# Performance work log

Hardware: AMD Instinct MI355X
Metric: run time of the kernel (lower is better)

## Reference

```python
import jax, jax.numpy as jnp
import numpy as np
from jax import lax

B, T, D = 4, 4096, 1024
H, d = 4, 64
EPS = 1e-6

def pos_unit(x):
    # positive feature map (elu+1) normalized to unit L2 norm along feature dim
    p = jax.nn.elu(x) + 1.0
    return p / (jnp.linalg.norm(p, axis=-1, keepdims=True) + EPS)

def setup_inputs() -> dict:
    key = jax.random.key(0)
    ks = jax.random.split(key, 5)
    s_in = 1.0 / np.sqrt(D)
    s_hd = 1.0 / np.sqrt(H * d)
    return {
        "x": jax.random.normal(ks[0], (B, T, D), dtype=jnp.float32),
        "Wq": jax.random.normal(ks[1], (H * d, D), dtype=jnp.float32) * s_in,
        "Wk": jax.random.normal(ks[2], (H * d, D), dtype=jnp.float32) * s_in,
        "Wv": jax.random.normal(ks[3], (H * d, D), dtype=jnp.float32) * s_in,
        "Wo": jax.random.normal(ks[4], (D, H * d), dtype=jnp.float32) * s_hd,
    }

def reference(x, Wq, Wk, Wv, Wo):
    Bx, Tx, Dx = x.shape
    q = (x @ Wq.T).reshape(Bx, Tx, H, d)
    k = (x @ Wk.T).reshape(Bx, Tx, H, d)
    v = (x @ Wv.T).reshape(Bx, Tx, H, d)
    q = pos_unit(q)
    k = pos_unit(k)
    # time-major for scan: [T, B, H, d]
    qT = jnp.transpose(q, (1, 0, 2, 3))
    kT = jnp.transpose(k, (1, 0, 2, 3))
    vT = jnp.transpose(v, (1, 0, 2, 3))
    kv0 = jnp.zeros((Bx, H, d, d), dtype=x.dtype)  # [B,H,j,d]
    kc0 = jnp.zeros((Bx, H, d), dtype=x.dtype)

    def step(carry, inp):
        kv_cum, k_cum = carry
        qt, kt, vt = inp  # each [B,H,d]
        kv_cum = kv_cum + jnp.einsum('bhd,bhj->bhjd', kt, vt)
        k_cum = k_cum + kt
        num = jnp.einsum('bhd,bhjd->bhj', qt, kv_cum)
        den = jnp.einsum('bhd,bhd->bh', qt, k_cum)[..., None] + EPS
        return (kv_cum, k_cum), num / den

    (kv_f, kc_f), yT = lax.scan(step, (kv0, kc0), (qT, kT, vT))
    y = jnp.transpose(yT, (1, 0, 2, 3)).reshape(Bx, Tx, H * d)
    y = y @ Wo.T
    return y, kv_f, kc_f
```

## Files before the change

### kernel.cpp

```cpp
#include <hip/hip_runtime.h>
#include <hip/hip_bf16.h>
#include <math.h>

#define T_SEQ   4096
#define NB      4
#define NH      4
#define DH      64
#define DM      1024
#define MR      16384
#define NQKV    768
#define CH      64
#define NCH     64
#define SST     4160
#define BHN     16

typedef __attribute__((ext_vector_type(4))) float          f32x4;
typedef __attribute__((ext_vector_type(8))) short          s16x8;
typedef __attribute__((ext_vector_type(4))) unsigned short u16x4;

__device__ __forceinline__ float bf2f(unsigned short u) {
  union { unsigned int i; float f; } c; c.i = ((unsigned int)u) << 16; return c.f;
}
__device__ __forceinline__ unsigned short f2bf(float f) {
  union { float f; unsigned int i; } c; c.f = f;
  unsigned int i = c.i;
  return (unsigned short)((i + 0x7fffu + ((i >> 16) & 1u)) >> 16);
}
__device__ __forceinline__ s16x8 pack8(f32x4 lo, f32x4 hi) {
  s16x8 r;
  r[0] = (short)f2bf(lo.x); r[1] = (short)f2bf(lo.y);
  r[2] = (short)f2bf(lo.z); r[3] = (short)f2bf(lo.w);
  r[4] = (short)f2bf(hi.x); r[5] = (short)f2bf(hi.y);
  r[6] = (short)f2bf(hi.z); r[7] = (short)f2bf(hi.w);
  return r;
}
__device__ __forceinline__ void gl_lds16(const unsigned short* g, unsigned short* l) {
  __builtin_amdgcn_global_load_lds(
      (const __attribute__((address_space(1))) unsigned int*)g,
      (__attribute__((address_space(3))) unsigned int*)l, 16, 0, 0);
}

__global__ __launch_bounds__(256) void convert_kernel(
    const float* __restrict__ X,
    const float* __restrict__ Wq, const float* __restrict__ Wk,
    const float* __restrict__ Wv,
    unsigned short* __restrict__ Xb, unsigned short* __restrict__ Wb)
{
  const long long NX = 16777216LL;
  const long long NW = 786432LL;
  const long long total = NX + NW;
  const long long stride = (long long)gridDim.x * 256 * 8;
  for (long long i = ((long long)blockIdx.x * 256 + threadIdx.x) * 8;
       i < total; i += stride) {
    const float* src;
    unsigned short* dst;
    if (i < NX) { src = X + i; dst = Xb + i; }
    else {
      const long long e = i - NX;
      const int w = (int)(e >> 18);
      const long long rr = e & 262143LL;
      src = (w == 0 ? Wq : w == 1 ? Wk : Wv) + rr;
      dst = Wb + e;
    }
    const f32x4 lo = *(const f32x4*)src;
    const f32x4 hi = *(const f32x4*)(src + 4);
    *(s16x8*)dst = pack8(lo, hi);
  }
}

__global__ __launch_bounds__(256) void convert_wo_kernel(
    const float* __restrict__ Wo, unsigned short* __restrict__ WoB)
{
  const int i = (blockIdx.x * 256 + threadIdx.x) * 8;
  const f32x4 lo = *(const f32x4*)(Wo + i);
  const f32x4 hi = *(const f32x4*)(Wo + i + 4);
  *(s16x8*)(WoB + i) = pack8(lo, hi);
}

__global__ __launch_bounds__(256, 2) void gemm_qkv_kernel(
    const unsigned short* __restrict__ Xb,
    const unsigned short* __restrict__ Wb,
    unsigned short* __restrict__ C)
{
  constexpr int K = DM;
  constexpr int N = NQKV;
  __shared__ __align__(16) unsigned short sA[2][128 * 32];
  __shared__ __align__(16) unsigned short sB[2][128 * 32];

  const int tid  = threadIdx.x;
  const int wave = tid >> 6;
  const int lane = tid & 63;
  const int quad = lane >> 4;
  const int l16  = lane & 15;
  const int wm = (wave >> 1) * 64;
  const int wn = (wave & 1) * 64;

  const int row0 = blockIdx.x * 128;
  const int bn   = blockIdx.y;
  const int srow = tid >> 2;
  const int scol = ((tid & 3) ^ (srow & 3)) * 8;
  const unsigned short* Ag = Xb + (size_t)(row0     + srow) * K + scol;
  const unsigned short* Bg = Wb + (size_t)(bn * 128 + srow) * K + scol;

  const int ra = (quad ^ (l16 & 3)) * 8;

  f32x4 acc[4][4];
  #pragma unroll
  for (int i = 0; i < 4; i++)
    #pragma unroll
    for (int j = 0; j < 4; j++) acc[i][j] = (f32x4){0.f, 0.f, 0.f, 0.f};

  gl_lds16(Ag,                       &sA[0][tid * 8]);
  gl_lds16(Ag + (size_t)64 * K,      &sA[0][tid * 8 + 2048]);
  gl_lds16(Bg,                       &sB[0][tid * 8]);
  gl_lds16(Bg + (size_t)64 * K,      &sB[0][tid * 8 + 2048]);
  gl_lds16(Ag + 32,                  &sA[1][tid * 8]);
  gl_lds16(Ag + 32 + (size_t)64 * K, &sA[1][tid * 8 + 2048]);
  gl_lds16(Bg + 32,                  &sB[1][tid * 8]);
  gl_lds16(Bg + 32 + (size_t)64 * K, &sB[1][tid * 8 + 2048]);
  asm volatile("s_waitcnt vmcnt(4)" ::: "memory");
  __builtin_amdgcn_sched_barrier(0);
  __builtin_amdgcn_s_barrier();

  int cur = 0;
  for (int kt = 0; kt < K; kt += 32) {
    s16x8 af[4], bw[4];
    #pragma unroll
    for (int i = 0; i < 4; i++)
      af[i] = *(const s16x8*)(&sA[cur][(wm + i * 16 + l16) * 32 + ra]);
    #pragma unroll
    for (int j = 0; j < 4; j++)
      bw[j] = *(const s16x8*)(&sB[cur][(wn + j * 16 + l16) * 32 + ra]);
    asm volatile("s_waitcnt lgkmcnt(0)" ::: "memory");
    __builtin_amdgcn_sched_barrier(0);
    __builtin_amdgcn_s_barrier();
    {
      const int ktp = (kt + 64 < K) ? (kt + 64) : (K - 32);
      gl_lds16(Ag + ktp,                  &sA[cur][tid * 8]);
      gl_lds16(Ag + ktp + (size_t)64 * K, &sA[cur][tid * 8 + 2048]);
      gl_lds16(Bg + ktp,                  &sB[cur][tid * 8]);
      gl_lds16(Bg + ktp + (size_t)64 * K, &sB[cur][tid * 8 + 2048]);
    }
    #pragma unroll
    for (int i = 0; i < 4; i++)
      #pragma unroll
      for (int j = 0; j < 4; j++)
        acc[i][j] = __builtin_amdgcn_mfma_f32_16x16x32_bf16(af[i], bw[j], acc[i][j], 0, 0, 0);
    asm volatile("s_waitcnt vmcnt(4)" ::: "memory");
    __builtin_amdgcn_sched_barrier(0);
    __builtin_amdgcn_s_barrier();
    cur ^= 1;
  }

  const int colb = bn * 128 + wn;
  if (bn < 4) {
    #pragma unroll
    for (int i = 0; i < 4; i++) {
      const int r = row0 + wm + i * 16 + quad * 4;
      #pragma unroll
      for (int g = 0; g < 4; g++) {
        float p[4];
        float ss = 0.f;
        #pragma unroll
        for (int j = 0; j < 4; j++) {
          const float a = acc[i][j][g];
          p[j] = a > 0.f ? a + 1.f : __expf(a);
          ss += p[j] * p[j];
        }
        ss += __shfl_xor(ss, 1, 64);
        ss += __shfl_xor(ss, 2, 64);
        ss += __shfl_xor(ss, 4, 64);
        ss += __shfl_xor(ss, 8, 64);
        const float inv = 1.f / (sqrtf(ss) + 1e-6f);
        #pragma unroll
        for (int j = 0; j < 4; j++)
          C[(size_t)(r + g) * N + colb + j * 16 + l16] = f2bf(p[j] * inv);
      }
    }
  } else {
    #pragma unroll
    for (int i = 0; i < 4; i++) {
      const int r = row0 + wm + i * 16 + quad * 4;
      #pragma unroll
      for (int j = 0; j < 4; j++) {
        const int cc = colb + j * 16 + l16;
        #pragma unroll
        for (int g = 0; g < 4; g++)
          C[(size_t)(r + g) * N + cc] = f2bf(acc[i][j][g]);
      }
    }
  }
}

__global__ __launch_bounds__(256, 2) void gemm_out_kernel(
    const unsigned short* __restrict__ Y,
    const unsigned short* __restrict__ WoB,
    float* __restrict__ Out)
{
  constexpr int K = 256;
  constexpr int N = DM;
  __shared__ __align__(16) unsigned short sA[128 * 32];
  __shared__ __align__(16) unsigned short sB[128 * 32];

  const int tid  = threadIdx.x;
  const int wave = tid >> 6;
  const int lane = tid & 63;
  const int quad = lane >> 4;
  const int l16  = lane & 15;
  const int wm = (wave >> 1) * 64;
  const int wn = (wave & 1) * 64;

  const int row0  = blockIdx.x * 128;
  const int bcol0 = blockIdx.y * 128;

  const int srow = tid >> 2;
  const int scol = ((tid & 3) ^ (srow & 3)) * 8;
  const unsigned short* Ag = Y   + (size_t)(row0  + srow) * K + scol;
  const unsigned short* Bg = WoB + (size_t)(bcol0 + srow) * K + scol;
  unsigned short* sAp = sA + tid * 8;
  unsigned short* sBp = sB + tid * 8;

  const int ra = (quad ^ (l16 & 3)) * 8;

  f32x4 acc[4][4];
  #pragma unroll
  for (int i = 0; i < 4; i++)
    #pragma unroll
    for (int j = 0; j < 4; j++) acc[i][j] = (f32x4){0.f, 0.f, 0.f, 0.f};

  for (int kt = 0; kt < K; kt += 32) {
    __syncthreads();
    gl_lds16(Ag + kt,                  sAp);
    gl_lds16(Ag + kt + (size_t)64 * K, sAp + 2048);
    gl_lds16(Bg + kt,                  sBp);
    gl_lds16(Bg + kt + (size_t)64 * K, sBp + 2048);
    __syncthreads();
    s16x8 af[4], bw[4];
    #pragma unroll
    for (int i = 0; i < 4; i++)
      af[i] = *(const s16x8*)(sA + (wm + i * 16 + l16) * 32 + ra);
    #pragma unroll
    for (int j = 0; j < 4; j++)
      bw[j] = *(const s16x8*)(sB + (wn + j * 16 + l16) * 32 + ra);
    #pragma unroll
    for (int i = 0; i < 4; i++)
      #pragma unroll
      for (int j = 0; j < 4; j++)
        acc[i][j] = __builtin_amdgcn_mfma_f32_16x16x32_bf16(af[i], bw[j], acc[i][j], 0, 0, 0);
  }

  #pragma unroll
  for (int i = 0; i < 4; i++) {
    const int r = row0 + wm + i * 16 + quad * 4;
    #pragma unroll
    for (int j = 0; j < 4; j++) {
      const int cc = bcol0 + wn + j * 16 + l16;
      #pragma unroll
      for (int g = 0; g < 4; g++)
        Out[(size_t)(r + g) * N + cc] = acc[i][j][g];
    }
  }
}

__global__ __launch_bounds__(256) void chunk_sums_kernel(
    const unsigned short* __restrict__ qkv,
    float* __restrict__ cs)
{
  const int blk = blockIdx.x;
  const int bh = blk >> 6, c = blk & 63;
  const int b = bh >> 2, h = bh & 3;
  __shared__ __align__(16) unsigned short sKt[64 * 64];
  __shared__ __align__(16) unsigned short sVt[64 * 64];
  __shared__ float sPart[4 * 64];
  const int wave = threadIdx.x >> 6, lane = threadIdx.x & 63;
  const int quad = lane >> 4, l16 = lane & 15;
  const size_t rowbase = ((size_t)b * T_SEQ + (size_t)c * CH) * NQKV + h * DH;

  float kacc = 0.f;
  #pragma unroll 4
  for (int tt = 0; tt < 16; tt++) {
    const int t = tt * 4 + wave;
    const unsigned short* r = qkv + rowbase + (size_t)t * NQKV;
    const unsigned short ku = r[256 + lane];
    const unsigned short vu = r[512 + lane];
    kacc += bf2f(ku);
    const int sw = (lane & 7) << 3;
    sKt[lane * 64 + (t ^ sw)] = ku;
    sVt[lane * 64 + (t ^ sw)] = vu;
  }
  sPart[wave * 64 + lane] = kacc;
  __syncthreads();

  const int wr = (wave >> 1) * 32;
  const int wc = (wave & 1) * 32;
  f32x4 acc[2][2];
  #pragma unroll
  for (int i = 0; i < 2; i++)
    #pragma unroll
    for (int j = 0; j < 2; j++) acc[i][j] = (f32x4){0.f, 0.f, 0.f, 0.f};

  #pragma unroll
  for (int ks = 0; ks < 2; ks++) {
    const int grp = ks * 4 + quad;
    s16x8 ak[2], bv[2];
    #pragma unroll
    for (int i = 0; i < 2; i++) {
      const int rk = wr + i * 16 + l16;
      ak[i] = *(const s16x8*)(sKt + rk * 64 + ((grp ^ (rk & 7)) << 3));
    }
    #pragma unroll
    for (int j = 0; j < 2; j++) {
      const int rj = wc + j * 16 + l16;
      bv[j] = *(const s16x8*)(sVt + rj * 64 + ((grp ^ (rj & 7)) << 3));
    }
    #pragma unroll
    for (int i = 0; i < 2; i++)
      #pragma unroll
      for (int j = 0; j < 2; j++)
        acc[i][j] = __builtin_amdgcn_mfma_f32_16x16x32_bf16(ak[i], bv[j], acc[i][j], 0, 0, 0);
  }

  float* o = cs + (size_t)blk * SST;
  #pragma unroll
  for (int i = 0; i < 2; i++)
    #pragma unroll
    for (int j = 0; j < 2; j++)
      #pragma unroll
      for (int g = 0; g < 4; g++) {
        const int dd = wr + i * 16 + quad * 4 + g;
        const int jj = wc + j * 16 + l16;
        o[dd * 64 + jj] = acc[i][j][g];
      }
  if (threadIdx.x < 64)
    o[4096 + threadIdx.x] = sPart[threadIdx.x] + sPart[64 + threadIdx.x]
                          + sPart[128 + threadIdx.x] + sPart[192 + threadIdx.x];
}

__global__ __launch_bounds__(256) void scan_kernel(
    float* __restrict__ cs, float* __restrict__ outTail)
{
  const int gid = blockIdx.x * 256 + threadIdx.x;
  const int bh = gid / SST;
  const int e  = gid - bh * SST;
  float run = 0.f;
  size_t idx = (size_t)bh * NCH * SST + e;
  for (int c = 0; c < NCH; c++, idx += SST) {
    const float v = cs[idx];
    cs[idx] = run;
    run += v;
  }
  if (e < 4096) {
    const int dd = e >> 6, j = e & 63;
    outTail[(size_t)bh * 4096 + j * 64 + dd] = run;
  } else {
    const int dd = e - 4096;
    outTail[BHN * 4096 + (size_t)bh * 64 + dd] = run;
  }
}

__global__ __launch_bounds__(256, 4) void chunk_out_kernel(
    const unsigned short* __restrict__ qkv,
    const float* __restrict__ st,
    unsigned short* __restrict__ yatt)
{
  const int blk = blockIdx.x;
  const int bh = blk >> 6;
  const int c  = blk & 63;
  const int b = bh >> 2, h = bh & 3;

  __shared__ __align__(16) unsigned short sQ [64 * 64];
  __shared__ __align__(16) unsigned short sKA[64 * 64];
  __shared__ __align__(16) unsigned short sVt[64 * 64];
  __shared__ __align__(16) unsigned short sSt[64 * 64];
  __shared__ float sKc[64];
  __shared__ float sDen[64];

  const int tid  = threadIdx.x;
  const int wave = tid >> 6, lane = tid & 63;
  const int quad = lane >> 4, l16 = lane & 15;
  const size_t rowbase = ((size_t)b * T_SEQ + (size_t)c * CH) * NQKV + h * DH;

  #pragma unroll
  for (int p = 0; p < 2; p++) {
    const int e  = p * 2048 + tid * 8;
    const int t  = e >> 6;
    const int c0 = e & 56;
    const int sc = c0 ^ ((t & 7) << 3);
    const unsigned short* src = qkv + rowbase + (size_t)t * NQKV + sc;
    gl_lds16(src,       sQ  + e);
    gl_lds16(src + 256, sKA + e);
  }
  #pragma unroll 4
  for (int tt = 0; tt < 16; tt++) {
    const int t = tt * 4 + wave;
    sVt[lane * 64 + (t ^ ((lane & 7) << 3))] =
        qkv[rowbase + (size_t)t * NQKV + 512 + lane];
  }
  const float* stp = st + (size_t)blk * SST;
  for (int i = tid; i < 1024; i += 256) {
    const f32x4 s4 = ((const f32x4*)stp)[i];
    const int d = i >> 4, j0 = (i & 15) << 2;
    #pragma unroll
    for (int g = 0; g < 4; g++) {
      const int j = j0 + g;
      sSt[j * 64 + (d ^ ((j & 7) << 3))] = f2bf(s4[g]);
    }
  }
  if (tid < 64) sKc[tid] = stp[4096 + tid];
  __syncthreads();

  const int wr = (wave >> 1) * 32;
  const int wc = (wave & 1) * 32;

  f32x4 accA[2][2];
  #pragma unroll
  for (int i = 0; i < 2; i++)
    #pragma unroll
    for (int j = 0; j < 2; j++) accA[i][j] = (f32x4){0.f, 0.f, 0.f, 0.f};

  #pragma unroll
  for (int ks = 0; ks < 2; ks++) {
    const int grp = ks * 4 + quad;
    s16x8 aq[2], bk[2];
    #pragma unroll
    for (int i = 0; i < 2; i++) {
      const int rq = wr + i * 16 + l16;
      aq[i] = *(const s16x8*)(sQ + rq * 64 + ((grp ^ (rq & 7)) << 3));
    }
    #pragma unroll
    for (int j = 0; j < 2; j++) {
      const int rk = wc + j * 16 + l16;
      bk[j] = *(const s16x8*)(sKA + rk * 64 + ((grp ^ (rk & 7)) << 3));
    }
    #pragma unroll
    for (int i = 0; i < 2; i++)
      #pragma unroll
      for (int j = 0; j < 2; j++)
        accA[i][j] = __builtin_amdgcn_mfma_f32_16x16x32_bf16(aq[i], bk[j], accA[i][j], 0, 0, 0);
  }
  __syncthreads();

  #pragma unroll
  for (int i = 0; i < 2; i++)
    #pragma unroll
    for (int j = 0; j < 2; j++)
      #pragma unroll
      for (int g = 0; g < 4; g++) {
        const int t = wr + i * 16 + quad * 4 + g;
        const int s = wc + j * 16 + l16;
        const float av = (s <= t) ? accA[i][j][g] : 0.f;
        sKA[t * 64 + (s ^ ((t & 7) << 3))] = f2bf(av);
      }
  __syncthreads();

  {
    const int t = tid >> 2, p = tid & 3;
    const int sw = (t & 7) << 3;
    float s = 0.f;
    #pragma unroll
    for (int e = 0; e < 16; e++) {
      const int d = p * 16 + e;
      s += bf2f(sKA[t * 64 + d]);
      s += bf2f(sQ[t * 64 + (d ^ sw)]) * sKc[d];
    }
    s += __shfl_xor(s, 1, 64);
    s += __shfl_xor(s, 2, 64);
    if (p == 0) sDen[t] = s + 1e-6f;
  }
  __syncthreads();

  f32x4 acc[2][2];
  #pragma unroll
  for (int i = 0; i < 2; i++)
    #pragma unroll
    for (int j = 0; j < 2; j++) acc[i][j] = (f32x4){0.f, 0.f, 0.f, 0.f};

  #pragma unroll
  for (int ks = 0; ks < 2; ks++) {
    const int grp = ks * 4 + quad;
    s16x8 aq[2], bs[2];
    #pragma unroll
    for (int i = 0; i < 2; i++) {
      const int rq = wr + i * 16 + l16;
      aq[i] = *(const s16x8*)(sQ + rq * 64 + ((grp ^ (rq & 7)) << 3));
    }
    #pragma unroll
    for (int j = 0; j < 2; j++) {
      const int rj = wc + j * 16 + l16;
      bs[j] = *(const s16x8*)(sSt + rj * 64 + ((grp ^ (rj & 7)) << 3));
    }
    #pragma unroll
    for (int i = 0; i < 2; i++)
      #pragma unroll
      for (int j = 0; j < 2; j++)
        acc[i][j] = __builtin_amdgcn_mfma_f32_16x16x32_bf16(aq[i], bs[j], acc[i][j], 0, 0, 0);
  }
  #pragma unroll
  for (int ks = 0; ks < 2; ks++) {
    const int grp = ks * 4 + quad;
    s16x8 aa[2], bv[2];
    #pragma unroll
    for (int i = 0; i < 2; i++) {
      const int rt = wr + i * 16 + l16;
      aa[i] = *(const s16x8*)(sKA + rt * 64 + ((grp ^ (rt & 7)) << 3));
    }
    #pragma unroll
    for (int j = 0; j < 2; j++) {
      const int rj = wc + j * 16 + l16;
      bv[j] = *(const s16x8*)(sVt + rj * 64 + ((grp ^ (rj & 7)) << 3));
    }
    #pragma unroll
    for (int i = 0; i < 2; i++)
      #pragma unroll
      for (int j = 0; j < 2; j++)
        acc[i][j] = __builtin_amdgcn_mfma_f32_16x16x32_bf16(aa[i], bv[j], acc[i][j], 0, 0, 0);
  }

  #pragma unroll
  for (int i = 0; i < 2; i++)
    #pragma unroll
    for (int g = 0; g < 4; g++) {
      const int t = wr + i * 16 + quad * 4 + g;
      const float inv = 1.f / sDen[t];
      #pragma unroll
      for (int j = 0; j < 2; j++) {
        const int jj = wc + j * 16 + l16;
        const size_t o = ((size_t)b * T_SEQ + (size_t)c * CH + t) * 256 + h * 64 + jj;
        yatt[o] = f2bf(acc[i][j][g] * inv);
      }
    }
}

extern "C" void kernel_launch(void* const* d_in, const int* in_sizes, int n_in,
                              void* d_out, int out_size, void* d_ws, size_t ws_size,
                              hipStream_t stream) {
  const float* X  = (const float*)d_in[0];
  const float* Wq = (const float*)d_in[1];
  const float* Wk = (const float*)d_in[2];
  const float* Wv = (const float*)d_in[3];
  const float* Wo = (const float*)d_in[4];
  float* out = (float*)d_out;

  unsigned short* qkvb = (unsigned short*)d_out;
  unsigned short* Xb   = (unsigned short*)((char*)d_out + 25165824ull);
  unsigned short* Wb   = Xb + 16777216;
  float* outTail = out + 16777216;
  float*          cs   = (float*)d_ws;
  unsigned short* yatt = (unsigned short*)((char*)d_ws + 17039360ull);
  unsigned short* WoB  = (unsigned short*)d_ws;

  convert_kernel   <<<4096,         256, 0, stream>>>(X, Wq, Wk, Wv, Xb, Wb);
  gemm_qkv_kernel  <<<dim3(128, 6), 256, 0, stream>>>(Xb, Wb, qkvb);
  chunk_sums_kernel<<<BHN * NCH,    256, 0, stream>>>(qkvb, cs);
  scan_kernel      <<<(BHN * SST) / 256, 256, 0, stream>>>(cs, outTail);
  chunk_out_kernel <<<BHN * NCH,    256, 0, stream>>>(qkvb, cs, yatt);
  convert_wo_kernel<<<128,          256, 0, stream>>>(Wo, WoB);
  gemm_out_kernel  <<<dim3(128, 8), 256, 0, stream>>>(yatt, WoB, out);
}
```

Baseline: 196.6 us.

## Enlarge QKV GEMM tiles to 256x256x64 with 512 threads and block swizzle

Restructures the QKV projection GEMM from 128x128 tiles with K-step 32 and 4 waves to 256x256 tiles with K-step 64 and 8 waves. Each wave now computes a 128x64 sub-tile. The grid becomes a 1D launch of 192 blocks, swizzled so neighbouring blocks share rows. The larger tiles are meant to raise operand reuse and cut global and LDS traffic per FLOP, and setprio is raised around the MFMA section. In exchange, shared memory grows to 128KB per block, register pressure rises with 32 accumulators per thread, and 192 blocks may leave the 256 CUs underfilled.

```diff
diff --git a/kernel.cpp b/kernel.cpp
--- a/kernel.cpp
+++ b/kernel.cpp
@@ -77,86 +77,110 @@
   *(s16x8*)(WoB + i) = pack8(lo, hi);
 }
 
-__global__ __launch_bounds__(256, 2) void gemm_qkv_kernel(
+__global__ __launch_bounds__(512, 2) void gemm_qkv_kernel(
     const unsigned short* __restrict__ Xb,
     const unsigned short* __restrict__ Wb,
     unsigned short* __restrict__ C)
 {
   constexpr int K = DM;
   constexpr int N = NQKV;
-  __shared__ __align__(16) unsigned short sA[2][128 * 32];
-  __shared__ __align__(16) unsigned short sB[2][128 * 32];
+  __shared__ __align__(16) unsigned short sA[2][256 * 64];
+  __shared__ __align__(16) unsigned short sB[2][256 * 64];
 
   const int tid  = threadIdx.x;
   const int wave = tid >> 6;
   const int lane = tid & 63;
   const int quad = lane >> 4;
   const int l16  = lane & 15;
-  const int wm = (wave >> 1) * 64;
-  const int wn = (wave & 1) * 64;
-
-  const int row0 = blockIdx.x * 128;
-  const int bn   = blockIdx.y;
-  const int srow = tid >> 2;
-  const int scol = ((tid & 3) ^ (srow & 3)) * 8;
-  const unsigned short* Ag = Xb + (size_t)(row0     + srow) * K + scol;
-  const unsigned short* Bg = Wb + (size_t)(bn * 128 + srow) * K + scol;
-
-  const int ra = (quad ^ (l16 & 3)) * 8;
-
-  f32x4 acc[4][4];
-  #pragma unroll
-  for (int i = 0; i < 4; i++)
+  const int wr = (wave >> 2) * 128;
+  const int wc = (wave & 3) * 64;
+
+  const int orig = blockIdx.x;
+  const int swz  = (orig & 7) * 24 + (orig >> 3);
+  const int bx   = swz / 3;
+  const int bn   = swz % 3;
+  const int row0 = bx * 256;
+
+  const unsigned short* Ab = Xb + (size_t)row0 * K;
+  const unsigned short* Bb = Wb + (size_t)(bn * 256) * K;
+
+  const int srow = tid >> 3;
+  const int sg   = tid & 7;
+  const int ssc  = (sg ^ (srow & 7)) << 3;
+
+  f32x4 acc[8][4];
+  #pragma unroll
+  for (int i = 0; i < 8; i++)
     #pragma unroll
     for (int j = 0; j < 4; j++) acc[i][j] = (f32x4){0.f, 0.f, 0.f, 0.f};
 
-  gl_lds16(Ag,                       &sA[0][tid * 8]);
-  gl_lds16(Ag + (size_t)64 * K,      &sA[0][tid * 8 + 2048]);
-  gl_lds16(Bg,                       &sB[0][tid * 8]);
-  gl_lds16(Bg + (size_t)64 * K,      &sB[0][tid * 8 + 2048]);
-  gl_lds16(Ag + 32,                  &sA[1][tid * 8]);
-  gl_lds16(Ag + 32 + (size_t)64 * K, &sA[1][tid * 8 + 2048]);
-  gl_lds16(Bg + 32,                  &sB[1][tid * 8]);
-  gl_lds16(Bg + 32 + (size_t)64 * K, &sB[1][tid * 8 + 2048]);
-  asm volatile("s_waitcnt vmcnt(4)" ::: "memory");
+#define STAGE_QKV(c, kt)                                                      \
+  {                                                                           \
+    _Pragma("unroll")                                                         \
+    for (int p = 0; p < 4; p++)                                               \
+      gl_lds16(Ab + (size_t)(p * 64 + srow) * K + (kt) + ssc,                 \
+               &sA[c][p * 4096 + tid * 8]);                                   \
+    _Pragma("unroll")                                                         \
+    for (int p = 0; p < 4; p++)                                               \
+      gl_lds16(Bb + (size_t)(p * 64 + srow) * K + (kt) + ssc,                 \
+               &sB[c][p * 4096 + tid * 8]);                                   \
+  }
+
+  STAGE_QKV(0, 0);
+  STAGE_QKV(1, 64);
+  asm volatile("s_waitcnt vmcnt(8)" ::: "memory");
   __builtin_amdgcn_sched_barrier(0);
   __builtin_amdgcn_s_barrier();
 
   int cur = 0;
-  for (int kt = 0; kt < K; kt += 32) {
-    s16x8 af[4], bw[4];
-    #pragma unroll
-    for (int i = 0; i < 4; i++)
-      af[i] = *(const s16x8*)(&sA[cur][(wm + i * 16 + l16) * 32 + ra]);
+  for (int kt = 0; kt < K; kt += 64) {
+    s16x8 bwf[4][2];
     #pragma unroll
     for (int j = 0; j < 4; j++)
-      bw[j] = *(const s16x8*)(&sB[cur][(wn + j * 16 + l16) * 32 + ra]);
+      #pragma unroll
+      for (int ks = 0; ks < 2; ks++) {
+        const int r = wc + j * 16 + l16;
+        bwf[j][ks] = *(const s16x8*)(&sB[cur][r * 64 + (((ks * 4 + quad) ^ (r & 7)) << 3)]);
+      }
+    __builtin_amdgcn_s_setprio(1);
+    #pragma unroll
+    for (int ph = 0; ph < 4; ph++) {
+      s16x8 afp[2][2];
+      #pragma unroll
+      for (int ii = 0; ii < 2; ii++)
+        #pragma unroll
+        for (int ks = 0; ks < 2; ks++) {
+          const int r = wr + (ph * 2 + ii) * 16 + l16;
+          afp[ii][ks] = *(const s16x8*)(&sA[cur][r * 64 + (((ks * 4 + quad) ^ (r & 7)) << 3)]);
+        }
+      #pragma unroll
+      for (int ii = 0; ii < 2; ii++)
+        #pragma unroll
+        for (int j = 0; j < 4; j++) {
+          acc[ph * 2 + ii][j] = __builtin_amdgcn_mfma_f32_16x16x32_bf16(
+              afp[ii][0], bwf[j][0], acc[ph * 2 + ii][j], 0, 0, 0);
+          acc[ph * 2 + ii][j] = __builtin_amdgcn_mfma_f32_16x16x32_bf16(
+              afp[ii][1], bwf[j][1], acc[ph * 2 + ii][j], 0, 0, 0);
+        }
+    }
+    __builtin_amdgcn_s_setprio(0);
     asm volatile("s_waitcnt lgkmcnt(0)" ::: "memory");
     __builtin_amdgcn_sched_barrier(0);
     __builtin_amdgcn_s_barrier();
-    {
-      const int ktp = (kt + 64 < K) ? (kt + 64) : (K - 32);
-      gl_lds16(Ag + ktp,                  &sA[cur][tid * 8]);
-      gl_lds16(Ag + ktp + (size_t)64 * K, &sA[cur][tid * 8 + 2048]);
-      gl_lds16(Bg + ktp,                  &sB[cur][tid * 8]);
-      gl_lds16(Bg + ktp + (size_t)64 * K, &sB[cur][tid * 8 + 2048]);
-    }
-    #pragma unroll
-    for (int i = 0; i < 4; i++)
-      #pragma unroll
-      for (int j = 0; j < 4; j++)
-        acc[i][j] = __builtin_amdgcn_mfma_f32_16x16x32_bf16(af[i], bw[j], acc[i][j], 0, 0, 0);
-    asm volatile("s_waitcnt vmcnt(4)" ::: "memory");
+    const int ktp = (kt + 128 < K) ? (kt + 128) : (K - 64);
+    STAGE_QKV(cur, ktp);
+    asm volatile("s_waitcnt vmcnt(8)" ::: "memory");
     __builtin_amdgcn_sched_barrier(0);
     __builtin_amdgcn_s_barrier();
     cur ^= 1;
   }
-
-  const int colb = bn * 128 + wn;
-  if (bn < 4) {
-    #pragma unroll
-    for (int i = 0; i < 4; i++) {
-      const int r = row0 + wm + i * 16 + quad * 4;
+#undef STAGE_QKV
+
+  const int colb = bn * 256 + wc;
+  if (bn < 2) {
+    #pragma unroll
+    for (int i = 0; i < 8; i++) {
+      const int r = row0 + wr + i * 16 + quad * 4;
       #pragma unroll
       for (int g = 0; g < 4; g++) {
         float p[4];
@@ -179,8 +203,8 @@
     }
   } else {
     #pragma unroll
-    for (int i = 0; i < 4; i++) {
-      const int r = row0 + wm + i * 16 + quad * 4;
+    for (int i = 0; i < 8; i++) {
+      const int r = row0 + wr + i * 16 + quad * 4;
       #pragma unroll
       for (int j = 0; j < 4; j++) {
         const int cc = colb + j * 16 + l16;
@@ -550,7 +574,7 @@
   unsigned short* WoB  = (unsigned short*)d_ws;
 
   convert_kernel   <<<4096,         256, 0, stream>>>(X, Wq, Wk, Wv, Xb, Wb);
-  gemm_qkv_kernel  <<<dim3(128, 6), 256, 0, stream>>>(Xb, Wb, qkvb);
+  gemm_qkv_kernel  <<<192,          512, 0, stream>>>(Xb, Wb, qkvb);
   chunk_sums_kernel<<<BHN * NCH,    256, 0, stream>>>(qkvb, cs);
   scan_kernel      <<<(BHN * SST) / 256, 256, 0, stream>>>(cs, outTail);
   chunk_out_kernel <<<BHN * NCH,    256, 0, stream>>>(qkvb, cs, yatt);
```

After: 204.5 us. +4.0%, slower.
